# Performance work log

Measured on AMD Instinct MI355X. Metric: run time of the kernel, lower is better.

## Reference

```python
import jax, jax.numpy as jnp
import numpy as np

MARGIN = 0.1   # init kwarg m
EPS = 1e-6     # CosineSimilarity eps
B, D, C = 8192, 1024, 14
LABEL_P = 0.1


def setup_inputs() -> dict:
    key = jax.random.key(0)
    k1, k2 = jax.random.split(key)
    pred = jax.random.normal(k1, (B, D), dtype=jnp.float32)
    gt = (jax.random.uniform(k2, (B, C)) < LABEL_P).astype(jnp.float32)
    return {"pred": pred, "gt": gt}


def _cos(x, y):
    # torch.nn.CosineSimilarity(dim=1, eps=1e-6): dot / max(||x||*||y||, eps)
    dot = jnp.sum(x * y, axis=1)
    nx = jnp.sqrt(jnp.sum(x * x, axis=1))
    ny = jnp.sqrt(jnp.sum(y * y, axis=1))
    return dot / jnp.maximum(nx * ny, EPS)


def reference(pred, gt):
    n = pred.shape[0]
    has = jnp.sum(gt, axis=1) > 0                      # [B] labeled rows (idxs_a)
    share = (gt @ gt.T) > 0                            # [B,B] rows sharing any label
    # Labeled anchor: positives = rows sharing a label (incl. self),
    #                 negatives = setdiff(idxs_a, rows_pos) U idxs_n == ~share row.
    # Unlabeled anchor: positives = unlabeled rows, negatives = labeled rows.
    pos_mask = jnp.where(has[:, None], share, ~has[None, :])
    neg_mask = jnp.where(has[:, None], ~share, has[None, :])
    # Uniform sampling among masked columns via Gumbel-max (replaces random.sample)
    kp, kn = jax.random.split(jax.random.key(42))
    NEG_INF = jnp.float32(-1e30)
    pos_idx = jnp.argmax(jnp.where(pos_mask, jax.random.gumbel(kp, (n, n)), NEG_INF), axis=1)
    neg_idx = jnp.argmax(jnp.where(neg_mask, jax.random.gumbel(kn, (n, n)), NEG_INF), axis=1)
    anchor = pred
    positive = pred[pos_idx]
    negative = pred[neg_idx]
    cos_v = _cos(anchor, positive) - _cos(anchor, negative) + MARGIN
    return jnp.mean(jnp.maximum(cos_v, 0.0))
```

## Files before the change

### kernel.cpp

```cpp
#include <hip/hip_runtime.h>
#include <hip/hip_bf16.h>
#include <stdint.h>

#define NB 8192
#define ND 1024
#define NC 14

static inline uint32_t rotl32h(uint32_t x, int r) { return (x << r) | (x >> (32 - r)); }
static void tf2x32_host(uint32_t k0, uint32_t k1, uint32_t x0, uint32_t x1,
                        uint32_t* o0, uint32_t* o1) {
  uint32_t ks[3] = { k0, k1, k0 ^ k1 ^ 0x1BD11BDAu };
  static const int R[8] = {13, 15, 26, 6, 17, 29, 16, 24};
  x0 += k0; x1 += k1;
  for (int g = 0; g < 5; ++g) {
    const int* rr = (g & 1) ? (R + 4) : R;
    for (int i = 0; i < 4; ++i) { x0 += x1; x1 = rotl32h(x1, rr[i]); x1 ^= x0; }
    x0 += ks[(g + 1) % 3];
    x1 += ks[(g + 2) % 3] + (uint32_t)(g + 1);
  }
  *o0 = x0; *o1 = x1;
}

__global__ void k_norm(const float* __restrict__ pred, const float* __restrict__ gt,
                       float* __restrict__ norm, uint32_t* __restrict__ lbits) {
  const int row = blockIdx.x;
  const float4* p = (const float4*)(pred + (size_t)row * ND);
  float4 v = p[threadIdx.x];
  float s = v.x * v.x + v.y * v.y + v.z * v.z + v.w * v.w;
#pragma unroll
  for (int o = 32; o > 0; o >>= 1) s += __shfl_down(s, o, 64);
  __shared__ float red[4];
  const int wave = threadIdx.x >> 6, lane = threadIdx.x & 63;
  if (lane == 0) red[wave] = s;
  unsigned long long b =
      __ballot((int)threadIdx.x < NC && gt[row * NC + (int)threadIdx.x] != 0.0f);
  __syncthreads();
  if (threadIdx.x == 0) {
    lbits[row] = (uint32_t)(b & 0x3FFFull);
    norm[row] = sqrtf(red[0] + red[1] + red[2] + red[3]);
  }
}

template <bool HAS>
__device__ __forceinline__ void sample_loop(
    const uint32_t* __restrict__ lbits, uint32_t bi, uint32_t fbase, uint32_t tid,
    uint32_t kp0, uint32_t kp1, uint32_t kps2,
    uint32_t kn0, uint32_t kn1, uint32_t kns2,
    uint32_t& bkP, uint32_t& bjP, uint32_t& bkN, uint32_t& bjN) {
#pragma unroll 8
  for (uint32_t k = 0; k < 32; ++k) {
    const uint32_t j = (k << 8) + tid;
    const uint32_t bj = lbits[j];
    const bool isPos = HAS ? ((bi & bj) != 0u) : (bj == 0u);
    const uint32_t K0 = isPos ? kp0 : kn0;
    const uint32_t K1 = isPos ? kp1 : kn1;
    const uint32_t KS2 = isPos ? kps2 : kns2;
    uint32_t x0 = K0;
    uint32_t x1 = fbase + j + K1;
#define TFR(r) { x0 += x1; x1 = (x1 << r) | (x1 >> (32 - r)); x1 ^= x0; }
    TFR(13) TFR(15) TFR(26) TFR(6)
    x0 += K1;  x1 += KS2 + 1u;
    TFR(17) TFR(29) TFR(16) TFR(24)
    x0 += KS2; x1 += K0 + 2u;
    TFR(13) TFR(15) TFR(26) TFR(6)
    x0 += K0;  x1 += K1 + 3u;
    TFR(17) TFR(29) TFR(16) TFR(24)
    x0 += K1;  x1 += KS2 + 4u;
    TFR(13) TFR(15) TFR(26) TFR(6)
    x0 += KS2; x1 += K0 + 5u;
#undef TFR
    const uint32_t key1 = ((x0 ^ x1) >> 9) + 1u;
    const bool gtP = isPos && (key1 > bkP);
    bkP = gtP ? key1 : bkP;
    bjP = gtP ? j : bjP;
    const bool gtN = (!isPos) && (key1 > bkN);
    bkN = gtN ? key1 : bkN;
    bjN = gtN ? j : bjN;
  }
}

__global__ void __launch_bounds__(256) k_sample(
    const uint32_t* __restrict__ lbits,
    uint32_t kp0, uint32_t kp1, uint32_t kps2,
    uint32_t kn0, uint32_t kn1, uint32_t kns2,
    int* __restrict__ pos_idx, int* __restrict__ neg_idx) {
  const int i = blockIdx.x;
  const uint32_t bi = lbits[i];
  const uint32_t fbase = (uint32_t)i << 13;
  const uint32_t tid = threadIdx.x;

  uint32_t bkP = 0u, bjP = 0u, bkN = 0u, bjN = 0u;
  if (bi != 0u)
    sample_loop<true>(lbits, bi, fbase, tid, kp0, kp1, kps2, kn0, kn1, kns2,
                      bkP, bjP, bkN, bjN);
  else
    sample_loop<false>(lbits, bi, fbase, tid, kp0, kp1, kps2, kn0, kn1, kns2,
                       bkP, bjP, bkN, bjN);

#pragma unroll
  for (int off = 32; off > 0; off >>= 1) {
    uint32_t k2 = __shfl_down(bkP, off, 64), j2 = __shfl_down(bjP, off, 64);
    if (k2 > bkP || (k2 == bkP && j2 < bjP)) { bkP = k2; bjP = j2; }
    k2 = __shfl_down(bkN, off, 64); j2 = __shfl_down(bjN, off, 64);
    if (k2 > bkN || (k2 == bkN && j2 < bjN)) { bkN = k2; bjN = j2; }
  }
  __shared__ uint32_t sk[2][4], sj[2][4];
  const int wave = (int)tid >> 6, lane = (int)tid & 63;
  if (lane == 0) { sk[0][wave] = bkP; sj[0][wave] = bjP; sk[1][wave] = bkN; sj[1][wave] = bjN; }
  __syncthreads();
  if (tid == 0) {
    uint32_t bk = sk[0][0], bj = sj[0][0];
#pragma unroll
    for (int w = 1; w < 4; ++w)
      if (sk[0][w] > bk || (sk[0][w] == bk && sj[0][w] < bj)) { bk = sk[0][w]; bj = sj[0][w]; }
    pos_idx[i] = (bk == 0u) ? 0 : (int)bj;
    bk = sk[1][0]; bj = sj[1][0];
#pragma unroll
    for (int w = 1; w < 4; ++w)
      if (sk[1][w] > bk || (sk[1][w] == bk && sj[1][w] < bj)) { bk = sk[1][w]; bj = sj[1][w]; }
    neg_idx[i] = (bk == 0u) ? 0 : (int)bj;
  }
}

__global__ void k_loss(const float* __restrict__ pred, const float* __restrict__ norm,
                       const int* __restrict__ pos_idx, const int* __restrict__ neg_idx,
                       float* __restrict__ losses) {
  const int i = blockIdx.x;
  const int p = pos_idx[i];
  const int n = neg_idx[i];
  const float4* A = (const float4*)(pred + (size_t)i * ND);
  const float4* P = (const float4*)(pred + (size_t)p * ND);
  const float4* Nn = (const float4*)(pred + (size_t)n * ND);
  float4 a = A[threadIdx.x], pp = P[threadIdx.x], nn = Nn[threadIdx.x];
  float dp = a.x * pp.x + a.y * pp.y + a.z * pp.z + a.w * pp.w;
  float dn = a.x * nn.x + a.y * nn.y + a.z * nn.z + a.w * nn.w;
#pragma unroll
  for (int o = 32; o > 0; o >>= 1) {
    dp += __shfl_down(dp, o, 64);
    dn += __shfl_down(dn, o, 64);
  }
  __shared__ float rdp[4], rdn[4];
  int wave = threadIdx.x >> 6, lane = threadIdx.x & 63;
  if (lane == 0) { rdp[wave] = dp; rdn[wave] = dn; }
  __syncthreads();
  if (threadIdx.x == 0) {
    float DP = rdp[0] + rdp[1] + rdp[2] + rdp[3];
    float DN = rdn[0] + rdn[1] + rdn[2] + rdn[3];
    float na = norm[i];
    float cp = DP / fmaxf(na * norm[p], 1e-6f);
    float cn = DN / fmaxf(na * norm[n], 1e-6f);
    losses[i] = fmaxf(cp - cn + 0.1f, 0.0f);
  }
}

__global__ void k_mean(const float* __restrict__ losses, float* __restrict__ out) {
  float s = 0.0f;
  for (int k = threadIdx.x; k < NB; k += 256) s += losses[k];
#pragma unroll
  for (int o = 32; o > 0; o >>= 1) s += __shfl_down(s, o, 64);
  __shared__ float red[4];
  int wave = threadIdx.x >> 6, lane = threadIdx.x & 63;
  if (lane == 0) red[wave] = s;
  __syncthreads();
  if (threadIdx.x == 0) out[0] = (red[0] + red[1] + red[2] + red[3]) / (float)NB;
}

extern "C" void kernel_launch(void* const* d_in, const int* in_sizes, int n_in,
                              void* d_out, int out_size, void* d_ws, size_t ws_size,
                              hipStream_t stream) {
  const float* pred = (const float*)d_in[0];
  const float* gt   = (const float*)d_in[1];
  float* out = (float*)d_out;

  char* ws = (char*)d_ws;
  uint32_t* lbits = (uint32_t*)(ws);
  float*    norms = (float*)(ws + 32768);
  int*      posi  = (int*)(ws + 65536);
  int*      negi  = (int*)(ws + 98304);
  float*    losses= (float*)(ws + 131072);

  uint32_t kp0, kp1, kn0, kn1;
  tf2x32_host(0u, 42u, 0u, 0u, &kp0, &kp1);
  tf2x32_host(0u, 42u, 0u, 1u, &kn0, &kn1);
  const uint32_t kps2 = kp0 ^ kp1 ^ 0x1BD11BDAu;
  const uint32_t kns2 = kn0 ^ kn1 ^ 0x1BD11BDAu;

  k_norm<<<NB, 256, 0, stream>>>(pred, gt, norms, lbits);
  k_sample<<<NB, 256, 0, stream>>>(lbits, kp0, kp1, kps2, kn0, kn1, kns2, posi, negi);
  k_loss<<<NB, 256, 0, stream>>>(pred, norms, posi, negi, losses);
  k_mean<<<1, 256, 0, stream>>>(losses, out);
}
```

Baseline: 241.8 us.

## Unify sampling branch via sentinel label bit, alignbit rotates, fuse mean via atomics

Unlabeled rows get a sentinel bit (0x4000) in the label mask, so a single bitwise AND gives the positive/negative test for both labeled and unlabeled anchors. This removes the templated branch split in the sampler. Threefry rotations use the amdgcn alignbit builtin, and keys are pinned in VGPRs with fbase pre-added. The final mean kernel is dropped in favour of a per-row atomicAdd into a memset output, which makes the float summation order nondeterministic and adds 8192 atomics to one address.

```diff
diff --git a/kernel.cpp b/kernel.cpp
--- a/kernel.cpp
+++ b/kernel.cpp
@@ -5,6 +5,8 @@
 #define NB 8192
 #define ND 1024
 #define NC 14
+
+#define ROTL(x, r) __builtin_amdgcn_alignbit((x), (x), 32u - (r))
 
 static inline uint32_t rotl32h(uint32_t x, int r) { return (x << r) | (x >> (32 - r)); }
 static void tf2x32_host(uint32_t k0, uint32_t k1, uint32_t x0, uint32_t x1,
@@ -22,7 +24,7 @@
 }
 
 __global__ void k_norm(const float* __restrict__ pred, const float* __restrict__ gt,
-                       float* __restrict__ norm, uint32_t* __restrict__ lbits) {
+                       float* __restrict__ norm, uint32_t* __restrict__ lbits2) {
   const int row = blockIdx.x;
   const float4* p = (const float4*)(pred + (size_t)row * ND);
   float4 v = p[threadIdx.x];
@@ -36,66 +38,62 @@
       __ballot((int)threadIdx.x < NC && gt[row * NC + (int)threadIdx.x] != 0.0f);
   __syncthreads();
   if (threadIdx.x == 0) {
-    lbits[row] = (uint32_t)(b & 0x3FFFull);
+    uint32_t m = (uint32_t)(b & 0x3FFFull);
+    lbits2[row] = m | ((m == 0u) ? 0x4000u : 0u);
     norm[row] = sqrtf(red[0] + red[1] + red[2] + red[3]);
   }
 }
 
-template <bool HAS>
-__device__ __forceinline__ void sample_loop(
-    const uint32_t* __restrict__ lbits, uint32_t bi, uint32_t fbase, uint32_t tid,
-    uint32_t kp0, uint32_t kp1, uint32_t kps2,
-    uint32_t kn0, uint32_t kn1, uint32_t kns2,
-    uint32_t& bkP, uint32_t& bjP, uint32_t& bkN, uint32_t& bjN) {
-#pragma unroll 8
-  for (uint32_t k = 0; k < 32; ++k) {
-    const uint32_t j = (k << 8) + tid;
-    const uint32_t bj = lbits[j];
-    const bool isPos = HAS ? ((bi & bj) != 0u) : (bj == 0u);
-    const uint32_t K0 = isPos ? kp0 : kn0;
-    const uint32_t K1 = isPos ? kp1 : kn1;
-    const uint32_t KS2 = isPos ? kps2 : kns2;
-    uint32_t x0 = K0;
-    uint32_t x1 = fbase + j + K1;
-#define TFR(r) { x0 += x1; x1 = (x1 << r) | (x1 >> (32 - r)); x1 ^= x0; }
-    TFR(13) TFR(15) TFR(26) TFR(6)
-    x0 += K1;  x1 += KS2 + 1u;
-    TFR(17) TFR(29) TFR(16) TFR(24)
-    x0 += KS2; x1 += K0 + 2u;
-    TFR(13) TFR(15) TFR(26) TFR(6)
-    x0 += K0;  x1 += K1 + 3u;
-    TFR(17) TFR(29) TFR(16) TFR(24)
-    x0 += K1;  x1 += KS2 + 4u;
-    TFR(13) TFR(15) TFR(26) TFR(6)
-    x0 += KS2; x1 += K0 + 5u;
-#undef TFR
-    const uint32_t key1 = ((x0 ^ x1) >> 9) + 1u;
-    const bool gtP = isPos && (key1 > bkP);
-    bkP = gtP ? key1 : bkP;
-    bjP = gtP ? j : bjP;
-    const bool gtN = (!isPos) && (key1 > bkN);
-    bkN = gtN ? key1 : bkN;
-    bjN = gtN ? j : bjN;
-  }
-}
-
 __global__ void __launch_bounds__(256) k_sample(
-    const uint32_t* __restrict__ lbits,
+    const uint32_t* __restrict__ lbits2,
     uint32_t kp0, uint32_t kp1, uint32_t kps2,
     uint32_t kn0, uint32_t kn1, uint32_t kns2,
     int* __restrict__ pos_idx, int* __restrict__ neg_idx) {
+  const uint32_t tid = threadIdx.x;
   const int i = blockIdx.x;
-  const uint32_t bi = lbits[i];
+  const uint32_t bi = lbits2[i];
   const uint32_t fbase = (uint32_t)i << 13;
-  const uint32_t tid = threadIdx.x;
+
+  uint32_t vkp0 = kp0, vkn0 = kn0, vkp1 = kp1, vkn1 = kn1;
+  uint32_t vkps2 = kps2, vkns2 = kns2;
+  uint32_t fkp1 = kp1 + fbase, fkn1 = kn1 + fbase;
+  asm("" : "+v"(vkp0), "+v"(vkn0), "+v"(vkp1), "+v"(vkn1),
+           "+v"(vkps2), "+v"(vkns2), "+v"(fkp1), "+v"(fkn1));
 
   uint32_t bkP = 0u, bjP = 0u, bkN = 0u, bjN = 0u;
-  if (bi != 0u)
-    sample_loop<true>(lbits, bi, fbase, tid, kp0, kp1, kps2, kn0, kn1, kns2,
-                      bkP, bjP, bkN, bjN);
-  else
-    sample_loop<false>(lbits, bi, fbase, tid, kp0, kp1, kps2, kn0, kn1, kns2,
-                       bkP, bjP, bkN, bjN);
+
+#pragma unroll 8
+  for (uint32_t k = 0; k < 32; ++k) {
+    const uint32_t jv = tid + (k << 8);
+    const uint32_t bj = lbits2[jv];
+    const uint32_t m = bi & bj;
+    const uint32_t s0 = m ? vkp0 : vkn0;
+    const uint32_t s1 = m ? vkp1 : vkn1;
+    const uint32_t s2 = m ? vkps2 : vkns2;
+    const uint32_t f1 = m ? fkp1 : fkn1;
+    uint32_t x0 = s0;
+    uint32_t x1 = f1 + jv;
+#define TFR(r) { x0 += x1; x1 = ROTL(x1, r); x1 ^= x0; }
+    TFR(13) TFR(15) TFR(26) TFR(6)
+    x0 += s1;  x1 += s2 + 1u;
+    TFR(17) TFR(29) TFR(16) TFR(24)
+    x0 += s2;  x1 += s0 + 2u;
+    TFR(13) TFR(15) TFR(26) TFR(6)
+    x0 += s0;  x1 += s1 + 3u;
+    TFR(17) TFR(29) TFR(16) TFR(24)
+    x0 += s1;  x1 += s2 + 4u;
+    TFR(13) TFR(15) TFR(26) TFR(6)
+    x0 += s2;  x1 += s0 + 5u;
+#undef TFR
+    const uint32_t key1 = ((x0 ^ x1) >> 9) + 1u;
+    const bool pos = (m != 0u);
+    const bool gtP = pos & (key1 > bkP);
+    bkP = gtP ? key1 : bkP;
+    bjP = gtP ? jv : bjP;
+    const bool gtN = (!pos) & (key1 > bkN);
+    bkN = gtN ? key1 : bkN;
+    bjN = gtN ? jv : bjN;
+  }
 
 #pragma unroll
   for (int off = 32; off > 0; off >>= 1) {
@@ -124,7 +122,7 @@
 
 __global__ void k_loss(const float* __restrict__ pred, const float* __restrict__ norm,
                        const int* __restrict__ pos_idx, const int* __restrict__ neg_idx,
-                       float* __restrict__ losses) {
+                       float* __restrict__ out) {
   const int i = blockIdx.x;
   const int p = pos_idx[i];
   const int n = neg_idx[i];
@@ -149,20 +147,9 @@
     float na = norm[i];
     float cp = DP / fmaxf(na * norm[p], 1e-6f);
     float cn = DN / fmaxf(na * norm[n], 1e-6f);
-    losses[i] = fmaxf(cp - cn + 0.1f, 0.0f);
+    float loss = fmaxf(cp - cn + 0.1f, 0.0f);
+    atomicAdd(out, loss * (1.0f / (float)NB));
   }
-}
-
-__global__ void k_mean(const float* __restrict__ losses, float* __restrict__ out) {
-  float s = 0.0f;
-  for (int k = threadIdx.x; k < NB; k += 256) s += losses[k];
-#pragma unroll
-  for (int o = 32; o > 0; o >>= 1) s += __shfl_down(s, o, 64);
-  __shared__ float red[4];
-  int wave = threadIdx.x >> 6, lane = threadIdx.x & 63;
-  if (lane == 0) red[wave] = s;
-  __syncthreads();
-  if (threadIdx.x == 0) out[0] = (red[0] + red[1] + red[2] + red[3]) / (float)NB;
 }
 
 extern "C" void kernel_launch(void* const* d_in, const int* in_sizes, int n_in,
@@ -177,7 +164,6 @@
   float*    norms = (float*)(ws + 32768);
   int*      posi  = (int*)(ws + 65536);
   int*      negi  = (int*)(ws + 98304);
-  float*    losses= (float*)(ws + 131072);
 
   uint32_t kp0, kp1, kn0, kn1;
   tf2x32_host(0u, 42u, 0u, 0u, &kp0, &kp1);
@@ -185,8 +171,8 @@
   const uint32_t kps2 = kp0 ^ kp1 ^ 0x1BD11BDAu;
   const uint32_t kns2 = kn0 ^ kn1 ^ 0x1BD11BDAu;
 
+  hipMemsetAsync(out, 0, sizeof(float), stream);
   k_norm<<<NB, 256, 0, stream>>>(pred, gt, norms, lbits);
   k_sample<<<NB, 256, 0, stream>>>(lbits, kp0, kp1, kps2, kn0, kn1, kns2, posi, negi);
-  k_loss<<<NB, 256, 0, stream>>>(pred, norms, posi, negi, losses);
-  k_mean<<<1, 256, 0, stream>>>(losses, out);
+  k_loss<<<NB, 256, 0, stream>>>(pred, norms, posi, negi, out);
 }
```

After: 333.5 us. 37.9% more time.
